# Optimization experiments

Measured on AMD Instinct MI355X. Metric: run time of the kernel, lower is better.

Reference implementation:

```python
import jax, jax.numpy as jnp
import numpy as np

B, CIN, COUT, K, H, W = 8, 256, 256, 3, 128, 128


def setup_inputs() -> dict:
    key = jax.random.key(0)
    k1, k2, k3 = jax.random.split(key, 3)
    return {
        "input_vector": jax.random.normal(k1, (B, CIN, H, W), dtype=jnp.float32),
        "style_vector": jax.random.normal(k2, (B, CIN), dtype=jnp.float32),
        "weight": jax.random.normal(k3, (COUT, CIN, K, K), dtype=jnp.float32),
    }


def reference(input_vector, style_vector, weight):
    b, cin, h, w = input_vector.shape
    cout, _, k, _ = weight.shape
    # per-sample modulated weights: (b, O, I, k, k)
    ws = weight[None, :, :, :, :] * style_vector[:, None, :, None, None]
    # NOTE: faithful to source - sum over dims [1,2,3] = (O, I, kh), NOT kw.
    demod = jax.lax.rsqrt(jnp.sum(ws * ws, axis=(1, 2, 3), keepdims=True) + 1e-8)  # (b,1,1,1,k)
    ws = (ws * demod).reshape(b * cout, cin, k, k)
    x = input_vector.reshape(1, b * cin, h, w)
    # get_same_padding(W, k, dilation=1, stride=1) = (k-1)//2
    pad = ((w - 1) * (1 - 1) + 1 * (k - 1)) // 2
    out = jax.lax.conv_general_dilated(
        x, ws,
        window_strides=(1, 1),
        padding=[(pad, pad), (pad, pad)],
        feature_group_count=b,
        dimension_numbers=("NCHW", "OIHW", "NCHW"),
    )
    out = out.reshape(b, cout, h, w)
    return jax.nn.leaky_relu(out, negative_slope=0.2)
```

## Files before the change

### kernel.cpp

```cpp
#include <hip/hip_runtime.h>
#include <hip/hip_bf16.h>

#define B_    8
#define CIN   256
#define COUT  256
#define H_    128
#define W_    128
#define HP    130
#define WP    130

#define RT    8
#define CT    32
#define OCT   128
#define XROWS 10
#define XCOLS 34
#define NSTEP 24

using bfrag = __attribute__((ext_vector_type(8))) short;
using f32x4 = __attribute__((ext_vector_type(4))) float;

__device__ __forceinline__ float leaky(float v) {
    return v >= 0.f ? v : 0.2f * v;
}

__device__ __forceinline__ unsigned short to_bf16(float v) {
    __hip_bfloat16 h = __float2bfloat16(v);
    return *(unsigned short*)&h;
}

__global__ void compute_S_kernel(const float* __restrict__ weight, float* __restrict__ S) {
    const int i = blockIdx.x;
    const int t = threadIdx.x;
    const float* wp = weight + ((size_t)t * CIN + i) * 9;
    float s0 = 0.f, s1 = 0.f, s2 = 0.f;
#pragma unroll
    for (int kh = 0; kh < 3; ++kh) {
        float a = wp[kh * 3 + 0], b = wp[kh * 3 + 1], c = wp[kh * 3 + 2];
        s0 = fmaf(a, a, s0); s1 = fmaf(b, b, s1); s2 = fmaf(c, c, s2);
    }
    __shared__ float red[3][256];
    red[0][t] = s0; red[1][t] = s1; red[2][t] = s2;
    __syncthreads();
    for (int off = 128; off > 0; off >>= 1) {
        if (t < off) {
            red[0][t] += red[0][t + off];
            red[1][t] += red[1][t + off];
            red[2][t] += red[2][t + off];
        }
        __syncthreads();
    }
    if (t == 0) {
        S[i * 3 + 0] = red[0][0];
        S[i * 3 + 1] = red[1][0];
        S[i * 3 + 2] = red[2][0];
    }
}

__global__ void compute_demod_kernel(const float* __restrict__ style,
                                     const float* __restrict__ S,
                                     float* __restrict__ demod) {
    const int b = blockIdx.x;
    const int t = threadIdx.x;
    float sv = style[b * CIN + t];
    float sv2 = sv * sv;
    float s0 = sv2 * S[t * 3 + 0];
    float s1 = sv2 * S[t * 3 + 1];
    float s2 = sv2 * S[t * 3 + 2];
    __shared__ float red[3][256];
    red[0][t] = s0; red[1][t] = s1; red[2][t] = s2;
    __syncthreads();
    for (int off = 128; off > 0; off >>= 1) {
        if (t < off) {
            red[0][t] += red[0][t + off];
            red[1][t] += red[1][t + off];
            red[2][t] += red[2][t + off];
        }
        __syncthreads();
    }
    if (t == 0) {
        demod[b * 3 + 0] = rsqrtf(red[0][0] + 1e-8f);
        demod[b * 3 + 1] = rsqrtf(red[1][0] + 1e-8f);
        demod[b * 3 + 2] = rsqrtf(red[2][0] + 1e-8f);
    }
}

__global__ void compute_wmodT_kernel(const float* __restrict__ weight,
                                     const float* __restrict__ style,
                                     const float* __restrict__ demod,
                                     unsigned short* __restrict__ wT) {
    const int bx = blockIdx.x;
    const int i  = threadIdx.x;
    const int o  = bx & (COUT - 1);
    const int j  = (bx >> 8) % 9;
    const int b  = bx / (9 * COUT);
    float w = weight[((size_t)o * CIN + i) * 9 + j];
    float m = style[b * CIN + i] * demod[b * 3 + (j % 3)];
    wT[(((size_t)(b * 9 + j) * COUT + o)) * CIN + i] = to_bf16(w * m);
}

__global__ __launch_bounds__(256) void transpose_kernel(const float* __restrict__ x,
                                                        unsigned short* __restrict__ xT) {
    const int bx = blockIdx.x;
    const int wtile = (bx & 3) * 32;
    const int itile = (bx >> 2) * 32;
    const int h = blockIdx.y;
    const int b = blockIdx.z;
    const int t = threadIdx.x;

    __shared__ float lt[32][33];

    {
        const int tw = t & 31, tr = t >> 5;
#pragma unroll
        for (int rr = 0; rr < 4; ++rr) {
            int il = tr + rr * 8;
            lt[il][tw] = x[(((size_t)b * CIN + itile + il) * H_ + h) * W_ + wtile + tw];
        }
    }
    __syncthreads();
    {
        const int il = t & 31, wr = t >> 5;
#pragma unroll
        for (int rr = 0; rr < 4; ++rr) {
            int wl = wr + rr * 8;
            xT[(((size_t)b * HP + (h + 1)) * WP + (wtile + wl + 1)) * CIN + itile + il] =
                to_bf16(lt[il][wl]);
        }
    }
}

__global__ __launch_bounds__(512) void conv_mfma_kernel(
    const unsigned short* __restrict__ xT,
    const unsigned short* __restrict__ wT,
    float* __restrict__ out)
{
    const int tid = threadIdx.x;
    const int b   = blockIdx.z;
    const int oc0 = blockIdx.y * OCT;
    const int ph  = blockIdx.x >> 2;
    const int pw  = blockIdx.x & 3;
    const int h0  = ph * RT, w0 = pw * CT;

    const int wid   = tid >> 6;
    const int lane  = tid & 63;
    const int wm    = wid >> 2;
    const int rn    = (wid >> 1) & 1;
    const int cn    = wid & 1;
    const int l15   = lane & 15;
    const int khalf = lane >> 4;

    __shared__ unsigned short lds_x[XROWS * XCOLS * 32];
    __shared__ unsigned short lds_a[2][3 * OCT * 32];

    const unsigned short* xb = xT + ((size_t)(b * HP + h0) * WP + w0) * CIN;
    const unsigned short* wb = wT + ((size_t)(b * 9) * COUT + oc0) * CIN;

    f32x4 acc[4][4];
#pragma unroll
    for (int m = 0; m < 4; ++m)
#pragma unroll
        for (int n = 0; n < 4; ++n) acc[m][n] = (f32x4){0.f, 0.f, 0.f, 0.f};

    auto stage_X = [&](int i0) {
        for (int idx = tid; idx < XROWS * XCOLS * 4; idx += 512) {
            int pix = idx >> 2, s = idx & 3;
            int r = pix / XCOLS, c = pix - r * XCOLS;
            int q = s ^ ((c >> 1) & 3);
            int4 v = *(const int4*)(xb + (size_t)(r * WP + c) * CIN + i0 + q * 8);
            *(int4*)&lds_x[pix * 32 + s * 8] = v;
        }
    };

    auto stage_A = [&](unsigned short* dst, const unsigned short* wsrc) {
#pragma unroll
        for (int j = 0; j < 3; ++j) {
            int c    = (wid * 3 + j) * 64 + lane;
            int slot = c & 3;
            int o    = (c >> 2) & 127;
            int kw   = c >> 9;
            const unsigned short* src = wsrc + ((size_t)kw * COUT + o) * CIN
                                        + ((slot ^ ((o >> 1) & 3)) << 3);
            __builtin_amdgcn_global_load_lds(
                (const __attribute__((address_space(1))) void*)src,
                (__attribute__((address_space(3))) void*)(dst + (wid * 3 + j) * 512),
                16, 0, 0);
        }
    };

    auto compute = [&](int kh, const unsigned short* abuf) {
#pragma unroll
        for (int kw = 0; kw < 3; ++kw) {
            bfrag aF[4];
#pragma unroll
            for (int m = 0; m < 4; ++m) {
                int oc = wm * 64 + m * 16 + l15;
                aF[m] = *(const bfrag*)&abuf[(kw * OCT + oc) * 32
                          + ((khalf ^ ((oc >> 1) & 3)) << 3)];
            }
#pragma unroll
            for (int n = 0; n < 4; ++n) {
                int row = rn * 4 + n + kh;
                int col = cn * 16 + l15 + kw;
                bfrag bF = *(const bfrag*)&lds_x[(row * XCOLS + col) * 32
                             + ((khalf ^ ((col >> 1) & 3)) << 3)];
#pragma unroll
                for (int m = 0; m < 4; ++m)
                    acc[m][n] = __builtin_amdgcn_mfma_f32_16x16x32_bf16(aF[m], bF, acc[m][n], 0, 0, 0);
            }
        }
    };

    stage_X(0);
    stage_A(lds_a[0], wb);
    __syncthreads();

#pragma unroll 1
    for (int s = 0; s < NSTEP; ++s) {
        const int kh = s % 3;
        if (s < NSTEP - 1) {
            const int sn  = s + 1;
            const int khn = sn % 3;
            const int i0n = (sn / 3) * 32;
            stage_A(lds_a[sn & 1], wb + (size_t)(khn * 3) * COUT * CIN + i0n);
        }
        compute(kh, lds_a[s & 1]);
        if (s < NSTEP - 1) {
            if (kh == 2) {
                __syncthreads();
                stage_X(((s + 1) / 3) * 32);
            }
            __syncthreads();
        }
    }

#pragma unroll
    for (int m = 0; m < 4; ++m) {
#pragma unroll
        for (int n = 0; n < 4; ++n) {
            int h = h0 + rn * 4 + n;
            int w = w0 + cn * 16 + l15;
#pragma unroll
            for (int r = 0; r < 4; ++r) {
                int oc = oc0 + wm * 64 + m * 16 + khalf * 4 + r;
                out[(((size_t)b * COUT + oc) * H_ + h) * W_ + w] = leaky(acc[m][n][r]);
            }
        }
    }
}

extern "C" void kernel_launch(void* const* d_in, const int* in_sizes, int n_in,
                              void* d_out, int out_size, void* d_ws, size_t ws_size,
                              hipStream_t stream) {
    const float* x      = (const float*)d_in[0];
    const float* style  = (const float*)d_in[1];
    const float* weight = (const float*)d_in[2];
    float* out = (float*)d_out;

    float* S     = (float*)d_ws;
    float* demod = (float*)((char*)d_ws + 4096);
    unsigned short* wT = (unsigned short*)((char*)d_ws + 8192);
    unsigned short* xT = (unsigned short*)((char*)d_ws + 9445376);

    hipMemsetAsync(xT, 0, (size_t)B_ * HP * WP * CIN * 2, stream);

    compute_S_kernel<<<CIN, 256, 0, stream>>>(weight, S);
    compute_demod_kernel<<<B_, 256, 0, stream>>>(style, S, demod);
    compute_wmodT_kernel<<<B_ * 9 * COUT, 256, 0, stream>>>(weight, style, demod, wT);
    transpose_kernel<<<dim3(32, H_, B_), 256, 0, stream>>>(x, xT);

    conv_mfma_kernel<<<dim3((H_ / RT) * (W_ / CT), COUT / OCT, B_), 512, 0, stream>>>(
        xT, wT, out);
}
```

Before: 212.5 us.

## Enlarge conv tile, async-pipeline X and weight loads, zero only padding border

```diff
diff --git a/kernel.cpp b/kernel.cpp
--- a/kernel.cpp
+++ b/kernel.cpp
@@ -9,15 +9,18 @@
 #define HP    130
 #define WP    130
 
-#define RT    8
-#define CT    32
 #define OCT   128
-#define XROWS 10
+#define TROWS 16
+#define TCOLS 32
+#define XROWS 18
 #define XCOLS 34
-#define NSTEP 24
+#define XCHUNKS_PAD 2560
 
 using bfrag = __attribute__((ext_vector_type(8))) short;
 using f32x4 = __attribute__((ext_vector_type(4))) float;
+
+#define ASM_VMCNT(n) asm volatile("s_waitcnt vmcnt(" #n ")" ::: "memory")
+#define ASM_LGKM0()  asm volatile("s_waitcnt lgkmcnt(0)" ::: "memory")
 
 __device__ __forceinline__ float leaky(float v) {
     return v >= 0.f ? v : 0.2f * v;
@@ -129,17 +132,35 @@
     }
 }
 
-__global__ __launch_bounds__(512) void conv_mfma_kernel(
+__global__ void zero_border_kernel(unsigned short* __restrict__ xT) {
+    const int b = blockIdx.x;
+    const int r = blockIdx.y;
+    const int t = threadIdx.x;
+    int npix, base, stride;
+    if (r == 0)      { npix = WP;  base = 0;                 stride = 1;  }
+    else if (r == 1) { npix = WP;  base = (HP - 1) * WP;     stride = 1;  }
+    else if (r == 2) { npix = 128; base = WP;                stride = WP; }
+    else             { npix = 128; base = WP + (WP - 1);     stride = WP; }
+    for (int idx = t; idx < npix * 32; idx += 256) {
+        int p = idx >> 5, q = idx & 31;
+        size_t off = ((size_t)b * HP * WP + base + (size_t)p * stride) * CIN;
+        *(int4*)((unsigned short*)xT + off + q * 8) = (int4){0, 0, 0, 0};
+    }
+}
+
+__global__ __launch_bounds__(512, 2) void conv_mfma_kernel(
     const unsigned short* __restrict__ xT,
     const unsigned short* __restrict__ wT,
     float* __restrict__ out)
 {
     const int tid = threadIdx.x;
-    const int b   = blockIdx.z;
-    const int oc0 = blockIdx.y * OCT;
-    const int ph  = blockIdx.x >> 2;
-    const int pw  = blockIdx.x & 3;
-    const int h0  = ph * RT, w0 = pw * CT;
+    const int lin = blockIdx.x + 32 * blockIdx.y + 64 * blockIdx.z;
+    const int b   = lin & 7;
+    const int rest = lin >> 3;
+    const int pxt  = rest & 31;
+    const int oc0  = (rest >> 5) * OCT;
+    const int ph = pxt >> 2, pw = pxt & 3;
+    const int h0 = ph * TROWS, w0 = pw * TCOLS;
 
     const int wid   = tid >> 6;
     const int lane  = tid & 63;
@@ -149,95 +170,130 @@
     const int l15   = lane & 15;
     const int khalf = lane >> 4;
 
-    __shared__ unsigned short lds_x[XROWS * XCOLS * 32];
-    __shared__ unsigned short lds_a[2][3 * OCT * 32];
+    __shared__ unsigned short lds_a[3][3 * OCT * 32];
+    __shared__ unsigned short lds_x[2][XCHUNKS_PAD * 8];
 
     const unsigned short* xb = xT + ((size_t)(b * HP + h0) * WP + w0) * CIN;
     const unsigned short* wb = wT + ((size_t)(b * 9) * COUT + oc0) * CIN;
 
-    f32x4 acc[4][4];
+    int offA[3];
+#pragma unroll
+    for (int j = 0; j < 3; ++j) {
+        int c    = (wid * 3 + j) * 64 + lane;
+        int slot = c & 3;
+        int o    = (c >> 2) & 127;
+        int kw   = c >> 9;
+        offA[j] = (kw * COUT + o) * CIN + ((slot ^ ((o >> 1) & 3)) << 3);
+    }
+    int offX[5];
+#pragma unroll
+    for (int j = 0; j < 5; ++j) {
+        int g  = (wid * 5 + j) * 64 + lane;
+        int gg = g < 2448 ? g : 0;
+        int pix = gg >> 2, slot = gg & 3;
+        int row = pix / XCOLS, col = pix - row * XCOLS;
+        offX[j] = (row * WP + col) * CIN + ((slot ^ ((col >> 1) & 3)) << 3);
+    }
+
+    f32x4 acc[4][8];
 #pragma unroll
     for (int m = 0; m < 4; ++m)
 #pragma unroll
-        for (int n = 0; n < 4; ++n) acc[m][n] = (f32x4){0.f, 0.f, 0.f, 0.f};
-
-    auto stage_X = [&](int i0) {
-        for (int idx = tid; idx < XROWS * XCOLS * 4; idx += 512) {
-            int pix = idx >> 2, s = idx & 3;
-            int r = pix / XCOLS, c = pix - r * XCOLS;
-            int q = s ^ ((c >> 1) & 3);
-            int4 v = *(const int4*)(xb + (size_t)(r * WP + c) * CIN + i0 + q * 8);
-            *(int4*)&lds_x[pix * 32 + s * 8] = v;
-        }
-    };
+        for (int n = 0; n < 8; ++n) acc[m][n] = (f32x4){0.f, 0.f, 0.f, 0.f};
 
     auto stage_A = [&](unsigned short* dst, const unsigned short* wsrc) {
 #pragma unroll
         for (int j = 0; j < 3; ++j) {
-            int c    = (wid * 3 + j) * 64 + lane;
-            int slot = c & 3;
-            int o    = (c >> 2) & 127;
-            int kw   = c >> 9;
-            const unsigned short* src = wsrc + ((size_t)kw * COUT + o) * CIN
-                                        + ((slot ^ ((o >> 1) & 3)) << 3);
             __builtin_amdgcn_global_load_lds(
-                (const __attribute__((address_space(1))) void*)src,
+                (const __attribute__((address_space(1))) void*)(wsrc + offA[j]),
                 (__attribute__((address_space(3))) void*)(dst + (wid * 3 + j) * 512),
                 16, 0, 0);
         }
     };
-
-    auto compute = [&](int kh, const unsigned short* abuf) {
-#pragma unroll
-        for (int kw = 0; kw < 3; ++kw) {
-            bfrag aF[4];
-#pragma unroll
-            for (int m = 0; m < 4; ++m) {
-                int oc = wm * 64 + m * 16 + l15;
-                aF[m] = *(const bfrag*)&abuf[(kw * OCT + oc) * 32
-                          + ((khalf ^ ((oc >> 1) & 3)) << 3)];
-            }
-#pragma unroll
-            for (int n = 0; n < 4; ++n) {
-                int row = rn * 4 + n + kh;
-                int col = cn * 16 + l15 + kw;
-                bfrag bF = *(const bfrag*)&lds_x[(row * XCOLS + col) * 32
-                             + ((khalf ^ ((col >> 1) & 3)) << 3)];
-#pragma unroll
-                for (int m = 0; m < 4; ++m)
-                    acc[m][n] = __builtin_amdgcn_mfma_f32_16x16x32_bf16(aF[m], bF, acc[m][n], 0, 0, 0);
-            }
+    auto stage_X = [&](unsigned short* dst, int i0) {
+#pragma unroll
+        for (int j = 0; j < 5; ++j) {
+            __builtin_amdgcn_global_load_lds(
+                (const __attribute__((address_space(1))) void*)(xb + offX[j] + i0),
+                (__attribute__((address_space(3))) void*)(dst + (wid * 5 + j) * 512),
+                16, 0, 0);
         }
     };
 
-    stage_X(0);
+#define COMPUTE(KH, ABUF, XBUF)                                                        \
+    {                                                                                  \
+        const unsigned short* _ab = (ABUF);                                            \
+        const unsigned short* _xb2 = (XBUF);                                           \
+        __builtin_amdgcn_s_setprio(1);                                                 \
+        _Pragma("unroll")                                                              \
+        for (int kw = 0; kw < 3; ++kw) {                                               \
+            bfrag aF[4];                                                               \
+            _Pragma("unroll")                                                          \
+            for (int m = 0; m < 4; ++m) {                                              \
+                int oc = wm * 64 + m * 16 + l15;                                       \
+                aF[m] = *(const bfrag*)&_ab[(kw * OCT + oc) * 32                       \
+                          + ((khalf ^ ((oc >> 1) & 3)) << 3)];                         \
+            }                                                                          \
+            _Pragma("unroll")                                                          \
+            for (int n = 0; n < 8; ++n) {                                              \
+                int row = rn * 8 + n + (KH);                                           \
+                int col = cn * 16 + l15 + kw;                                          \
+                bfrag bF = *(const bfrag*)&_xb2[(row * XCOLS + col) * 32               \
+                             + ((khalf ^ ((col >> 1) & 3)) << 3)];                     \
+                _Pragma("unroll")                                                      \
+                for (int m = 0; m < 4; ++m)                                            \
+                    acc[m][n] = __builtin_amdgcn_mfma_f32_16x16x32_bf16(               \
+                        aF[m], bF, acc[m][n], 0, 0, 0);                                \
+            }                                                                          \
+        }                                                                              \
+        __builtin_amdgcn_s_setprio(0);                                                 \
+    }
+
+    const size_t KHS = (size_t)3 * COUT * CIN;
+
     stage_A(lds_a[0], wb);
-    __syncthreads();
+    stage_A(lds_a[1], wb + KHS);
+    stage_X(lds_x[0], 0);
+    ASM_VMCNT(0);
+    __builtin_amdgcn_s_barrier();
+    __builtin_amdgcn_sched_barrier(0);
 
 #pragma unroll 1
-    for (int s = 0; s < NSTEP; ++s) {
-        const int kh = s % 3;
-        if (s < NSTEP - 1) {
-            const int sn  = s + 1;
-            const int khn = sn % 3;
-            const int i0n = (sn / 3) * 32;
-            stage_A(lds_a[sn & 1], wb + (size_t)(khn * 3) * COUT * CIN + i0n);
-        }
-        compute(kh, lds_a[s & 1]);
-        if (s < NSTEP - 1) {
-            if (kh == 2) {
-                __syncthreads();
-                stage_X(((s + 1) / 3) * 32);
-            }
-            __syncthreads();
-        }
-    }
+    for (int c = 0; c < 8; ++c) {
+        const int i0  = c * 32;
+        const int i0n = ((c + 1) & 7) * 32;
+        unsigned short* xcur = lds_x[c & 1];
+        unsigned short* xnxt = lds_x[(c + 1) & 1];
+
+        stage_A(lds_a[2], wb + 2 * KHS + i0);
+        COMPUTE(0, lds_a[0], xcur);
+        ASM_LGKM0();
+        ASM_VMCNT(3);
+        __builtin_amdgcn_s_barrier();
+        __builtin_amdgcn_sched_barrier(0);
+
+        stage_A(lds_a[0], wb + i0n);
+        stage_X(xnxt, i0n);
+        COMPUTE(1, lds_a[1], xcur);
+        ASM_LGKM0();
+        ASM_VMCNT(8);
+        __builtin_amdgcn_s_barrier();
+        __builtin_amdgcn_sched_barrier(0);
+
+        stage_A(lds_a[1], wb + KHS + i0n);
+        COMPUTE(2, lds_a[2], xcur);
+        ASM_LGKM0();
+        ASM_VMCNT(3);
+        __builtin_amdgcn_s_barrier();
+        __builtin_amdgcn_sched_barrier(0);
+    }
+    ASM_VMCNT(0);
 
 #pragma unroll
     for (int m = 0; m < 4; ++m) {
 #pragma unroll
-        for (int n = 0; n < 4; ++n) {
-            int h = h0 + rn * 4 + n;
+        for (int n = 0; n < 8; ++n) {
+            int h = h0 + rn * 8 + n;
             int w = w0 + cn * 16 + l15;
 #pragma unroll
             for (int r = 0; r < 4; ++r) {
@@ -246,6 +302,7 @@
             }
         }
     }
+#undef COMPUTE
 }
 
 extern "C" void kernel_launch(void* const* d_in, const int* in_sizes, int n_in,
@@ -261,13 +318,11 @@
     unsigned short* wT = (unsigned short*)((char*)d_ws + 8192);
     unsigned short* xT = (unsigned short*)((char*)d_ws + 9445376);
 
-    hipMemsetAsync(xT, 0, (size_t)B_ * HP * WP * CIN * 2, stream);
-
     compute_S_kernel<<<CIN, 256, 0, stream>>>(weight, S);
     compute_demod_kernel<<<B_, 256, 0, stream>>>(style, S, demod);
     compute_wmodT_kernel<<<B_ * 9 * COUT, 256, 0, stream>>>(weight, style, demod, wT);
     transpose_kernel<<<dim3(32, H_, B_), 256, 0, stream>>>(x, xT);
-
-    conv_mfma_kernel<<<dim3((H_ / RT) * (W_ / CT), COUT / OCT, B_), 512, 0, stream>>>(
-        xT, wT, out);
-}
+    zero_border_kernel<<<dim3(B_, 4), 256, 0, stream>>>(xT);
+
+    conv_mfma_kernel<<<dim3(32, 2, B_), 512, 0, stream>>>(xT, wT, out);
+}
```

After: 208.5 us. No clear change (-1.9%).

## Restructure conv kernel: 4 waves, larger per-wave tiles, async LDS loads, border-only zeroing

Applied to the files above, without the earlier changes.

```diff
diff --git a/kernel.cpp b/kernel.cpp
--- a/kernel.cpp
+++ b/kernel.cpp
@@ -9,15 +9,21 @@
 #define HP    130
 #define WP    130
 
-#define RT    8
-#define CT    32
 #define OCT   128
+#define TROWS 8
+#define TCOLS 32
 #define XROWS 10
 #define XCOLS 34
+#define XCH   1360
+#define XCHP  1536
 #define NSTEP 24
+#define KHS   ((size_t)3 * COUT * CIN)
 
 using bfrag = __attribute__((ext_vector_type(8))) short;
 using f32x4 = __attribute__((ext_vector_type(4))) float;
+
+#define ASM_VMCNT(n) asm volatile("s_waitcnt vmcnt(" #n ")" ::: "memory")
+#define ASM_LGKM0()  asm volatile("s_waitcnt lgkmcnt(0)" ::: "memory")
 
 __device__ __forceinline__ float leaky(float v) {
     return v >= 0.f ? v : 0.2f * v;
@@ -129,116 +135,157 @@
     }
 }
 
-__global__ __launch_bounds__(512) void conv_mfma_kernel(
+__global__ void zero_border_kernel(unsigned short* __restrict__ xT) {
+    const int b = blockIdx.x;
+    const int r = blockIdx.y;
+    const int t = threadIdx.x;
+    int npix, base, stride;
+    if (r == 0)      { npix = WP;  base = 0;                 stride = 1;  }
+    else if (r == 1) { npix = WP;  base = (HP - 1) * WP;     stride = 1;  }
+    else if (r == 2) { npix = 128; base = WP;                stride = WP; }
+    else             { npix = 128; base = WP + (WP - 1);     stride = WP; }
+    for (int idx = t; idx < npix * 32; idx += 256) {
+        int p = idx >> 5, q = idx & 31;
+        size_t off = ((size_t)b * HP * WP + base + (size_t)p * stride) * CIN;
+        *(int4*)((unsigned short*)xT + off + q * 8) = (int4){0, 0, 0, 0};
+    }
+}
+
+__global__ __launch_bounds__(256, 2) void conv_mfma_kernel(
     const unsigned short* __restrict__ xT,
     const unsigned short* __restrict__ wT,
     float* __restrict__ out)
 {
     const int tid = threadIdx.x;
-    const int b   = blockIdx.z;
-    const int oc0 = blockIdx.y * OCT;
-    const int ph  = blockIdx.x >> 2;
-    const int pw  = blockIdx.x & 3;
-    const int h0  = ph * RT, w0 = pw * CT;
+    const int lin = blockIdx.x;
+    const int b    = lin & 7;
+    const int rest = lin >> 3;
+    const int oc0  = (rest & 1) * OCT;
+    const int w0   = ((rest >> 1) & 3) * TCOLS;
+    const int h0   = (rest >> 3) * TROWS;
 
     const int wid   = tid >> 6;
     const int lane  = tid & 63;
-    const int wm    = wid >> 2;
-    const int rn    = (wid >> 1) & 1;
-    const int cn    = wid & 1;
+    const int wm    = wid >> 1;
+    const int cw    = wid & 1;
     const int l15   = lane & 15;
     const int khalf = lane >> 4;
 
-    __shared__ unsigned short lds_x[XROWS * XCOLS * 32];
     __shared__ unsigned short lds_a[2][3 * OCT * 32];
+    __shared__ unsigned short lds_x[XCHP * 8];
 
     const unsigned short* xb = xT + ((size_t)(b * HP + h0) * WP + w0) * CIN;
     const unsigned short* wb = wT + ((size_t)(b * 9) * COUT + oc0) * CIN;
 
-    f32x4 acc[4][4];
+    int offA[6];
+#pragma unroll
+    for (int j = 0; j < 6; ++j) {
+        int c    = (wid * 6 + j) * 64 + lane;
+        int slot = c & 3;
+        int o    = (c >> 2) & 127;
+        int kw   = c >> 9;
+        offA[j] = (kw * COUT + o) * CIN + ((slot ^ ((o >> 1) & 3)) << 3);
+    }
+    int offX[6];
+#pragma unroll
+    for (int j = 0; j < 6; ++j) {
+        int g  = (wid * 6 + j) * 64 + lane;
+        int gg = g < XCH ? g : 0;
+        int pix = gg >> 2, slot = gg & 3;
+        int row = pix / XCOLS, col = pix - row * XCOLS;
+        offX[j] = (row * WP + col) * CIN + ((slot ^ ((col >> 1) & 3)) << 3);
+    }
+
+    f32x4 acc[4][8];
 #pragma unroll
     for (int m = 0; m < 4; ++m)
 #pragma unroll
-        for (int n = 0; n < 4; ++n) acc[m][n] = (f32x4){0.f, 0.f, 0.f, 0.f};
-
+        for (int n = 0; n < 8; ++n) acc[m][n] = (f32x4){0.f, 0.f, 0.f, 0.f};
+
+    auto stage_A = [&](unsigned short* dst, const unsigned short* wsrc) {
+#pragma unroll
+        for (int j = 0; j < 6; ++j) {
+            __builtin_amdgcn_global_load_lds(
+                (const __attribute__((address_space(1))) void*)(wsrc + offA[j]),
+                (__attribute__((address_space(3))) void*)(dst + (wid * 6 + j) * 512),
+                16, 0, 0);
+        }
+    };
     auto stage_X = [&](int i0) {
-        for (int idx = tid; idx < XROWS * XCOLS * 4; idx += 512) {
-            int pix = idx >> 2, s = idx & 3;
-            int r = pix / XCOLS, c = pix - r * XCOLS;
-            int q = s ^ ((c >> 1) & 3);
-            int4 v = *(const int4*)(xb + (size_t)(r * WP + c) * CIN + i0 + q * 8);
-            *(int4*)&lds_x[pix * 32 + s * 8] = v;
+#pragma unroll
+        for (int j = 0; j < 6; ++j) {
+            __builtin_amdgcn_global_load_lds(
+                (const __attribute__((address_space(1))) void*)(xb + offX[j] + i0),
+                (__attribute__((address_space(3))) void*)(lds_x + (wid * 6 + j) * 512),
+                16, 0, 0);
         }
     };
 
-    auto stage_A = [&](unsigned short* dst, const unsigned short* wsrc) {
-#pragma unroll
-        for (int j = 0; j < 3; ++j) {
-            int c    = (wid * 3 + j) * 64 + lane;
-            int slot = c & 3;
-            int o    = (c >> 2) & 127;
-            int kw   = c >> 9;
-            const unsigned short* src = wsrc + ((size_t)kw * COUT + o) * CIN
-                                        + ((slot ^ ((o >> 1) & 3)) << 3);
-            __builtin_amdgcn_global_load_lds(
-                (const __attribute__((address_space(1))) void*)src,
-                (__attribute__((address_space(3))) void*)(dst + (wid * 3 + j) * 512),
-                16, 0, 0);
-        }
-    };
-
-    auto compute = [&](int kh, const unsigned short* abuf) {
+    auto compute = [&](int kh, const unsigned short* ab) {
+        __builtin_amdgcn_s_setprio(1);
 #pragma unroll
         for (int kw = 0; kw < 3; ++kw) {
             bfrag aF[4];
 #pragma unroll
             for (int m = 0; m < 4; ++m) {
                 int oc = wm * 64 + m * 16 + l15;
-                aF[m] = *(const bfrag*)&abuf[(kw * OCT + oc) * 32
+                aF[m] = *(const bfrag*)&ab[(kw * OCT + oc) * 32
                           + ((khalf ^ ((oc >> 1) & 3)) << 3)];
             }
 #pragma unroll
-            for (int n = 0; n < 4; ++n) {
-                int row = rn * 4 + n + kh;
-                int col = cn * 16 + l15 + kw;
+            for (int n = 0; n < 8; ++n) {
+                int row = n + kh;
+                int col = cw * 16 + l15 + kw;
                 bfrag bF = *(const bfrag*)&lds_x[(row * XCOLS + col) * 32
                              + ((khalf ^ ((col >> 1) & 3)) << 3)];
 #pragma unroll
                 for (int m = 0; m < 4; ++m)
-                    acc[m][n] = __builtin_amdgcn_mfma_f32_16x16x32_bf16(aF[m], bF, acc[m][n], 0, 0, 0);
+                    acc[m][n] = __builtin_amdgcn_mfma_f32_16x16x32_bf16(
+                        aF[m], bF, acc[m][n], 0, 0, 0);
             }
         }
+        __builtin_amdgcn_s_setprio(0);
     };
 
     stage_X(0);
     stage_A(lds_a[0], wb);
-    __syncthreads();
+    ASM_VMCNT(0);
+    __builtin_amdgcn_s_barrier();
+    __builtin_amdgcn_sched_barrier(0);
 
 #pragma unroll 1
     for (int s = 0; s < NSTEP; ++s) {
-        const int kh = s % 3;
+        const int c  = s / 3;
+        const int kh = s - 3 * c;
+        unsigned short* acur = lds_a[s & 1];
+        unsigned short* anxt = lds_a[(s + 1) & 1];
+
         if (s < NSTEP - 1) {
-            const int sn  = s + 1;
-            const int khn = sn % 3;
-            const int i0n = (sn / 3) * 32;
-            stage_A(lds_a[sn & 1], wb + (size_t)(khn * 3) * COUT * CIN + i0n);
-        }
-        compute(kh, lds_a[s & 1]);
-        if (s < NSTEP - 1) {
-            if (kh == 2) {
-                __syncthreads();
-                stage_X(((s + 1) / 3) * 32);
-            }
-            __syncthreads();
-        }
+            const int sn = s + 1;
+            const int cn2 = sn / 3;
+            const int khn = sn - 3 * cn2;
+            stage_A(anxt, wb + (size_t)khn * KHS + cn2 * 32);
+        }
+        if (kh == 0) {
+            ASM_VMCNT(6);
+            __builtin_amdgcn_s_barrier();
+            __builtin_amdgcn_sched_barrier(0);
+        }
+        compute(kh, acur);
+        ASM_LGKM0();
+        ASM_VMCNT(0);
+        __builtin_amdgcn_s_barrier();
+        __builtin_amdgcn_sched_barrier(0);
+        if (kh == 2 && s < NSTEP - 1)
+            stage_X((c + 1) * 32);
     }
 
 #pragma unroll
     for (int m = 0; m < 4; ++m) {
 #pragma unroll
-        for (int n = 0; n < 4; ++n) {
-            int h = h0 + rn * 4 + n;
-            int w = w0 + cn * 16 + l15;
+        for (int n = 0; n < 8; ++n) {
+            int h = h0 + n;
+            int w = w0 + cw * 16 + l15;
 #pragma unroll
             for (int r = 0; r < 4; ++r) {
                 int oc = oc0 + wm * 64 + m * 16 + khalf * 4 + r;
@@ -261,13 +308,11 @@
     unsigned short* wT = (unsigned short*)((char*)d_ws + 8192);
     unsigned short* xT = (unsigned short*)((char*)d_ws + 9445376);
 
-    hipMemsetAsync(xT, 0, (size_t)B_ * HP * WP * CIN * 2, stream);
-
     compute_S_kernel<<<CIN, 256, 0, stream>>>(weight, S);
     compute_demod_kernel<<<B_, 256, 0, stream>>>(style, S, demod);
     compute_wmodT_kernel<<<B_ * 9 * COUT, 256, 0, stream>>>(weight, style, demod, wT);
     transpose_kernel<<<dim3(32, H_, B_), 256, 0, stream>>>(x, xT);
-
-    conv_mfma_kernel<<<dim3((H_ / RT) * (W_ / CT), COUT / OCT, B_), 512, 0, stream>>>(
-        xT, wT, out);
-}
+    zero_border_kernel<<<dim3(B_, 4), 256, 0, stream>>>(xT);
+
+    conv_mfma_kernel<<<dim3(1024), 256, 0, stream>>>(xT, wT, out);
+}
```

Result: faster. 188.7 us (-11.2%).
